# Kernel tuning notes

Measured on AMD Instinct MI355X. Metric: run time of the kernel, lower is better.

Reference implementation:

```python
import jax, jax.numpy as jnp
import numpy as np

B, S, D, H = 2, 2048, 1024, 16
DH = D // H
NEG = jnp.float32(-1e30)


def setup_inputs() -> dict:
    key = jax.random.key(0)
    ks = jax.random.split(key, 5)
    x = jax.random.normal(ks[0], (B, S, D), dtype=jnp.float32)
    # causal mask: attn_mask == 0 means blocked (matches masked_fill(attn_mask == 0))
    attn_mask = jnp.tril(jnp.ones((S, S), dtype=jnp.int32))
    key_padding_mask = jnp.zeros((B, S), dtype=bool)  # True = pad (none here)
    sd = 1.0 / np.sqrt(D)
    W_qkv = jax.random.normal(ks[1], (D, 3 * D), dtype=jnp.float32) * sd
    b_qkv = jnp.zeros((3 * D,), dtype=jnp.float32)
    W_proj = jax.random.normal(ks[2], (D, D), dtype=jnp.float32) * sd
    b_proj = jnp.zeros((D,), dtype=jnp.float32)
    return {"x": x, "W_qkv": W_qkv, "b_qkv": b_qkv, "W_proj": W_proj,
            "b_proj": b_proj, "attn_mask": attn_mask,
            "key_padding_mask": key_padding_mask}


def reference(x, W_qkv, b_qkv, W_proj, b_proj, attn_mask, key_padding_mask):
    scale = jnp.float32(DH) ** -0.5
    qkv = (x @ W_qkv + b_qkv).reshape(B, S, 3, H, DH)
    qkv = jnp.transpose(qkv, (2, 0, 3, 1, 4))  # (3, B, H, S, DH)
    q, k, v = qkv[0], qkv[1], qkv[2]
    attn = jnp.einsum("bhqd,bhkd->bhqk", q, k) * scale  # (B,H,S,S)
    # key padding mask: True -> -inf on that key column
    attn = jnp.where(key_padding_mask[:, None, None, :], NEG, attn)
    # attn mask: 0 -> blocked
    attn = jnp.where(attn_mask[None, None, :, :] == 0, NEG, attn)
    attn = jax.nn.softmax(attn, axis=-1)
    out = jnp.einsum("bhqk,bhkd->bhqd", attn, v)
    out = jnp.transpose(out, (0, 2, 1, 3)).reshape(B, S, D)
    return out @ W_proj + b_proj
```

## Files before the change

### kernel.cpp

```cpp
#include <hip/hip_runtime.h>


typedef __bf16 bf16;
typedef bf16 bf16x4 __attribute__((ext_vector_type(4)));
typedef bf16 bf16x8 __attribute__((ext_vector_type(8)));
typedef float f32x4 __attribute__((ext_vector_type(4)));

#define S_LEN 2048
#define DMODEL 1024
#define NHEAD 16
#define DHEAD 64

__device__ __forceinline__ void async_ld16(void* lds, const void* g) {
  __builtin_amdgcn_global_load_lds(
      (const __attribute__((address_space(1))) unsigned int*)g,
      (__attribute__((address_space(3))) unsigned int*)lds, 16, 0, 0);
}

__global__ __launch_bounds__(256) void convert_f32_bf16(
    const float* __restrict__ in, bf16* __restrict__ out, int n4) {
  int i = blockIdx.x * blockDim.x + threadIdx.x;
  if (i < n4) {
    float4 v = ((const float4*)in)[i];
    bf16x4 o;
    o[0] = (bf16)v.x; o[1] = (bf16)v.y; o[2] = (bf16)v.z; o[3] = (bf16)v.w;
    *(bf16x4*)(&out[4 * i]) = o;
  }
}

__global__ __launch_bounds__(256) void transpose_f32_bf16(
    const float* __restrict__ in, bf16* __restrict__ out, int R, int C) {
  __shared__ float t[32][33];
  int bc = blockIdx.x * 32, br = blockIdx.y * 32;
  int tx = threadIdx.x, ty = threadIdx.y;
#pragma unroll
  for (int i = 0; i < 32; i += 8)
    t[ty + i][tx] = in[(size_t)(br + ty + i) * C + bc + tx];
  __syncthreads();
#pragma unroll
  for (int i = 0; i < 32; i += 8)
    out[(size_t)(bc + ty + i) * R + br + tx] = (bf16)t[tx][ty + i];
}

__global__ __launch_bounds__(256) void gemm_qkv(
    const bf16* __restrict__ A, const bf16* __restrict__ Bt,
    const float* __restrict__ bias, bf16* __restrict__ Oq,
    bf16* __restrict__ Ok, bf16* __restrict__ Ov, int Ksz) {
  __shared__ bf16 As[128 * 32];
  __shared__ bf16 Bs[128 * 32];
  const int tid = threadIdx.x, lane = tid & 63, w = tid >> 6;
  const int wm = (w >> 1) * 64, wn = (w & 1) * 64;
  const int lr = lane & 15, kg = lane >> 4;
  const int m0 = blockIdx.y * 128, n0 = blockIdx.x * 128;

  f32x4 acc[4][4] = {};

  for (int k0 = 0; k0 < Ksz; k0 += 32) {
#pragma unroll
    for (int i = 0; i < 2; ++i) {
      int seg = tid + i * 256;
      int row = seg >> 2, cs = (seg & 3) * 8;
      async_ld16(&As[row * 32 + cs], &A[(size_t)(m0 + row) * Ksz + k0 + cs]);
      async_ld16(&Bs[row * 32 + cs], &Bt[(size_t)(n0 + row) * Ksz + k0 + cs]);
    }
    __syncthreads();
    bf16x8 af[4], bfr[4];
#pragma unroll
    for (int i = 0; i < 4; ++i)
      af[i] = *(const bf16x8*)(&As[(wm + i * 16 + lr) * 32 + kg * 8]);
#pragma unroll
    for (int j = 0; j < 4; ++j)
      bfr[j] = *(const bf16x8*)(&Bs[(wn + j * 16 + lr) * 32 + kg * 8]);
#pragma unroll
    for (int i = 0; i < 4; ++i)
#pragma unroll
      for (int j = 0; j < 4; ++j)
        acc[i][j] = __builtin_amdgcn_mfma_f32_16x16x32_bf16(af[i], bfr[j], acc[i][j], 0, 0, 0);
    __syncthreads();
  }

  const int rbase = kg * 4;
#pragma unroll
  for (int i = 0; i < 4; ++i) {
#pragma unroll
    for (int j = 0; j < 4; ++j) {
      int ncol = n0 + wn + j * 16 + lr;
      float bv = bias[ncol];
#pragma unroll
      for (int r = 0; r < 4; ++r) {
        int m = m0 + wm + i * 16 + rbase + r;
        float v = acc[i][j][r] + bv;
        int t = ncol >> 10, rem = ncol & 1023;
        int h = rem >> 6, d = rem & 63;
        int s = m & 2047;
        size_t hb = (size_t)((m >> 11) * NHEAD + h) * S_LEN;
        if (t == 0)      Oq[(hb + s) * DHEAD + d] = (bf16)v;
        else if (t == 1) Ok[(hb + s) * DHEAD + d] = (bf16)v;
        else             Ov[hb * DHEAD + (size_t)d * S_LEN + s] = (bf16)v;
      }
    }
  }
}

__global__ __launch_bounds__(256) void gemm_proj(
    const bf16* __restrict__ A, const bf16* __restrict__ Bt,
    const float* __restrict__ bias, float* __restrict__ Of,
    int Ksz, int Nsz) {
  __shared__ bf16 As[64 * 32];
  __shared__ bf16 Bs[128 * 32];
  const int tid = threadIdx.x, lane = tid & 63, w = tid >> 6;
  const int wm = (w >> 1) * 32, wn = (w & 1) * 64;
  const int lr = lane & 15, kg = lane >> 4;
  const int m0 = blockIdx.y * 64, n0 = blockIdx.x * 128;

  f32x4 acc[2][4] = {};

  for (int k0 = 0; k0 < Ksz; k0 += 32) {
    {
      int row = tid >> 2, cs = (tid & 3) * 8;
      async_ld16(&As[row * 32 + cs], &A[(size_t)(m0 + row) * Ksz + k0 + cs]);
    }
#pragma unroll
    for (int i = 0; i < 2; ++i) {
      int seg = tid + i * 256;
      int row = seg >> 2, cs = (seg & 3) * 8;
      async_ld16(&Bs[row * 32 + cs], &Bt[(size_t)(n0 + row) * Ksz + k0 + cs]);
    }
    __syncthreads();
    bf16x8 af[2], bfr[4];
#pragma unroll
    for (int i = 0; i < 2; ++i)
      af[i] = *(const bf16x8*)(&As[(wm + i * 16 + lr) * 32 + kg * 8]);
#pragma unroll
    for (int j = 0; j < 4; ++j)
      bfr[j] = *(const bf16x8*)(&Bs[(wn + j * 16 + lr) * 32 + kg * 8]);
#pragma unroll
    for (int i = 0; i < 2; ++i)
#pragma unroll
      for (int j = 0; j < 4; ++j)
        acc[i][j] = __builtin_amdgcn_mfma_f32_16x16x32_bf16(af[i], bfr[j], acc[i][j], 0, 0, 0);
    __syncthreads();
  }

  const int rbase = kg * 4;
#pragma unroll
  for (int i = 0; i < 2; ++i) {
#pragma unroll
    for (int j = 0; j < 4; ++j) {
      int ncol = n0 + wn + j * 16 + lr;
      float bv = bias[ncol];
#pragma unroll
      for (int r = 0; r < 4; ++r) {
        int m = m0 + wm + i * 16 + rbase + r;
        Of[(size_t)m * Nsz + ncol] = acc[i][j][r] + bv;
      }
    }
  }
}

__global__ __launch_bounds__(256) void attn_kernel(
    const bf16* __restrict__ Q, const bf16* __restrict__ K,
    const bf16* __restrict__ Vtg, bf16* __restrict__ O) {
  __shared__ bf16 Ks[128 * 72];
  __shared__ bf16 Vt[64 * 136];
  __shared__ bf16 Pt[4][16 * 136];

  const int tid = threadIdx.x, lane = tid & 63, w = tid >> 6;
  const int lr = lane & 15, quad = lane >> 4;
  const int bh = blockIdx.y;
  const int b = bh >> 4, h = bh & 15;
  const bf16* Qp = Q + (size_t)bh * S_LEN * DHEAD;
  const bf16* Kp = K + (size_t)bh * S_LEN * DHEAD;
  const bf16* Vp = Vtg + (size_t)bh * S_LEN * DHEAD;

  const float qs = 0.125f * 1.44269504f;

  for (int seg = 0; seg < 2; ++seg) {
    const int qt = seg ? (31 - (int)blockIdx.x) : (int)blockIdx.x;
    const int q0 = qt * 64;
    const int qrow = q0 + w * 16;

    bf16x8 q0r = *(const bf16x8*)(Qp + (size_t)(qrow + lr) * DHEAD + quad * 8);
    bf16x8 q1r = *(const bf16x8*)(Qp + (size_t)(qrow + lr) * DHEAD + 32 + quad * 8);
    bf16x8 qf0, qf1;
#pragma unroll
    for (int e = 0; e < 8; ++e) {
      qf0[e] = (bf16)((float)q0r[e] * qs);
      qf1[e] = (bf16)((float)q1r[e] * qs);
    }

    f32x4 acc[4] = {};
    float m_i = -1e30f, l_i = 0.f;

    const int ktiles = (q0 + 63) / 128 + 1;
    for (int kt = 0; kt < ktiles; ++kt) {
      const int kb = kt * 128;
#pragma unroll
      for (int i = 0; i < 4; ++i) {
        int sg = tid + i * 256;
        int krow = sg >> 3, kc = (sg & 7) * 8;
        *(bf16x8*)(&Ks[krow * 72 + kc]) =
            *(const bf16x8*)(&Kp[(size_t)(kb + krow) * DHEAD + kc]);
        int vd = sg >> 4, vs = (sg & 15) * 8;
        *(bf16x8*)(&Vt[vd * 136 + vs]) =
            *(const bf16x8*)(&Vp[(size_t)vd * S_LEN + kb + vs]);
      }
      __syncthreads();

      f32x4 sc[8];
#pragma unroll
      for (int ct = 0; ct < 8; ++ct) {
        bf16x8 kf0 = *(const bf16x8*)(&Ks[(ct * 16 + lr) * 72 + quad * 8]);
        bf16x8 kf1 = *(const bf16x8*)(&Ks[(ct * 16 + lr) * 72 + 32 + quad * 8]);
        f32x4 a = {};
        a = __builtin_amdgcn_mfma_f32_16x16x32_bf16(kf0, qf0, a, 0, 0, 0);
        a = __builtin_amdgcn_mfma_f32_16x16x32_bf16(kf1, qf1, a, 0, 0, 0);
        sc[ct] = a;
      }

      const bool full = (kb + 127) <= qrow;
      float pmax = -1e30f;
      if (full) {
#pragma unroll
        for (int ct = 0; ct < 8; ++ct)
#pragma unroll
          for (int r = 0; r < 4; ++r) pmax = fmaxf(pmax, sc[ct][r]);
      } else {
        const int qg = qrow + lr;
#pragma unroll
        for (int ct = 0; ct < 8; ++ct)
#pragma unroll
          for (int r = 0; r < 4; ++r) {
            int key = kb + ct * 16 + quad * 4 + r;
            if (key > qg) sc[ct][r] = -1e30f;
            pmax = fmaxf(pmax, sc[ct][r]);
          }
      }
      pmax = fmaxf(pmax, __shfl_xor(pmax, 16));
      pmax = fmaxf(pmax, __shfl_xor(pmax, 32));

      float mn = fmaxf(m_i, pmax);
      float alpha = __builtin_amdgcn_exp2f(m_i - mn);
      m_i = mn;
      float psum = 0.f;
#pragma unroll
      for (int ct = 0; ct < 8; ++ct)
#pragma unroll
        for (int r = 0; r < 4; ++r) {
          float p = __builtin_amdgcn_exp2f(sc[ct][r] - mn);
          sc[ct][r] = p;
          psum += p;
        }
      psum += __shfl_xor(psum, 16);
      psum += __shfl_xor(psum, 32);
      l_i = l_i * alpha + psum;
#pragma unroll
      for (int nt = 0; nt < 4; ++nt)
#pragma unroll
        for (int r = 0; r < 4; ++r) acc[nt][r] *= alpha;

#pragma unroll
      for (int ct = 0; ct < 8; ++ct) {
        bf16x4 pk;
#pragma unroll
        for (int r = 0; r < 4; ++r) pk[r] = (bf16)sc[ct][r];
        *(bf16x4*)(&Pt[w][lr * 136 + ct * 16 + quad * 4]) = pk;
      }

#pragma unroll
      for (int k0 = 0; k0 < 4; ++k0) {
        bf16x8 pf = *(const bf16x8*)(&Pt[w][lr * 136 + k0 * 32 + quad * 8]);
#pragma unroll
        for (int nt = 0; nt < 4; ++nt) {
          bf16x8 vf = *(const bf16x8*)(&Vt[(nt * 16 + lr) * 136 + k0 * 32 + quad * 8]);
          acc[nt] = __builtin_amdgcn_mfma_f32_16x16x32_bf16(vf, pf, acc[nt], 0, 0, 0);
        }
      }
      __syncthreads();
    }

    float inv = 1.f / l_i;
    size_t base = ((size_t)(b * S_LEN + qrow + lr)) * DMODEL + h * DHEAD;
#pragma unroll
    for (int nt = 0; nt < 4; ++nt) {
      bf16x4 ov;
#pragma unroll
      for (int r = 0; r < 4; ++r) ov[r] = (bf16)(acc[nt][r] * inv);
      *(bf16x4*)(&O[base + nt * 16 + quad * 4]) = ov;
    }
  }
}

extern "C" void kernel_launch(void* const* d_in, const int* in_sizes, int n_in,
                              void* d_out, int out_size, void* d_ws, size_t ws_size,
                              hipStream_t stream) {
  (void)in_sizes; (void)n_in; (void)out_size; (void)ws_size;
  const float* x     = (const float*)d_in[0];
  const float* Wqkv  = (const float*)d_in[1];
  const float* bqkv  = (const float*)d_in[2];
  const float* Wproj = (const float*)d_in[3];
  const float* bproj = (const float*)d_in[4];
  float* out = (float*)d_out;

  char* ws = (char*)d_ws;
  bf16* Xb  = (bf16*)(ws + 0);
  bf16* AO  = (bf16*)(ws + 0);
  bf16* Wtq = (bf16*)(ws + 8388608);
  bf16* Wtp = (bf16*)(ws + 16777216);
  bf16* Qb  = (bf16*)(ws + 18874368);
  bf16* Kb  = (bf16*)(ws + 27262976);
  bf16* Vtg = (bf16*)(ws + 35651584);

  convert_f32_bf16<<<4096, 256, 0, stream>>>(x, Xb, 4194304 / 4);
  transpose_f32_bf16<<<dim3(96, 32), dim3(32, 8), 0, stream>>>(Wqkv, Wtq, 1024, 3072);
  transpose_f32_bf16<<<dim3(32, 32), dim3(32, 8), 0, stream>>>(Wproj, Wtp, 1024, 1024);
  gemm_qkv<<<dim3(24, 32), 256, 0, stream>>>(Xb, Wtq, bqkv, Qb, Kb, Vtg, 1024);
  attn_kernel<<<dim3(16, 32), 256, 0, stream>>>(Qb, Kb, Vtg, AO);
  gemm_proj<<<dim3(8, 64), 256, 0, stream>>>(AO, Wtp, bproj, out, 1024, 1024);
}
```

Baseline: 215.6 us.

## Merge prep kernels, compute softmax row sums via MFMA, swizzle attention grid

Three conversion and transpose launches are merged into one prep kernel with a block-range dispatch, removing two launch overheads. In attention, the row-sum of probabilities is now computed by an extra MFMA against a ones-row appended to the V tile in LDS, replacing the per-tile cross-lane shuffle reductions. The attention grid is also flattened and remapped so groups of 8 heads share query-tile indices, which may improve L2 locality. The row-sum MFMA adds LDS usage and one MFMA per k-step, and it accumulates the bf16-rounded probabilities, which changes numerics slightly.

```diff
diff --git a/kernel.cpp b/kernel.cpp
--- a/kernel.cpp
+++ b/kernel.cpp
@@ -17,22 +17,30 @@
       (__attribute__((address_space(3))) unsigned int*)lds, 16, 0, 0);
 }
 
-__global__ __launch_bounds__(256) void convert_f32_bf16(
-    const float* __restrict__ in, bf16* __restrict__ out, int n4) {
-  int i = blockIdx.x * blockDim.x + threadIdx.x;
-  if (i < n4) {
-    float4 v = ((const float4*)in)[i];
+__global__ __launch_bounds__(256) void prep_kernel(
+    const float* __restrict__ x, const float* __restrict__ Wq,
+    const float* __restrict__ Wp, bf16* __restrict__ Xb,
+    bf16* __restrict__ Wtq, bf16* __restrict__ Wtp) {
+  __shared__ float t[32][33];
+  const int bid = blockIdx.x, tid = threadIdx.x;
+  if (bid < 4096) {
+    int i = bid * 256 + tid;
+    float4 v = ((const float4*)x)[i];
     bf16x4 o;
     o[0] = (bf16)v.x; o[1] = (bf16)v.y; o[2] = (bf16)v.z; o[3] = (bf16)v.w;
-    *(bf16x4*)(&out[4 * i]) = o;
-  }
-}
-
-__global__ __launch_bounds__(256) void transpose_f32_bf16(
-    const float* __restrict__ in, bf16* __restrict__ out, int R, int C) {
-  __shared__ float t[32][33];
-  int bc = blockIdx.x * 32, br = blockIdx.y * 32;
-  int tx = threadIdx.x, ty = threadIdx.y;
+    *(bf16x4*)(&Xb[4 * i]) = o;
+    return;
+  }
+  const float* in; bf16* out; int R, C, bx, by;
+  if (bid < 7168) {
+    int b = bid - 4096; in = Wq; out = Wtq; R = 1024; C = 3072;
+    bx = b % 96; by = b / 96;
+  } else {
+    int b = bid - 7168; in = Wp; out = Wtp; R = 1024; C = 1024;
+    bx = b % 32; by = b / 32;
+  }
+  int tx = tid & 31, ty = tid >> 5;
+  int bc = bx * 32, br = by * 32;
 #pragma unroll
   for (int i = 0; i < 32; i += 8)
     t[ty + i][tx] = in[(size_t)(br + ty + i) * C + bc + tx];
@@ -162,21 +170,29 @@
     const bf16* __restrict__ Q, const bf16* __restrict__ K,
     const bf16* __restrict__ Vtg, bf16* __restrict__ O) {
   __shared__ bf16 Ks[128 * 72];
-  __shared__ bf16 Vt[64 * 136];
+  __shared__ bf16 Vt[80 * 136];
   __shared__ bf16 Pt[4][16 * 136];
 
   const int tid = threadIdx.x, lane = tid & 63, w = tid >> 6;
   const int lr = lane & 15, quad = lane >> 4;
-  const int bh = blockIdx.y;
+  const int flat = blockIdx.x;
+  const int p = (flat >> 3) & 15;
+  const int bh = (flat & 7) + ((flat >> 7) << 3);
   const int b = bh >> 4, h = bh & 15;
   const bf16* Qp = Q + (size_t)bh * S_LEN * DHEAD;
   const bf16* Kp = K + (size_t)bh * S_LEN * DHEAD;
   const bf16* Vp = Vtg + (size_t)bh * S_LEN * DHEAD;
 
+  for (int i = tid; i < 16 * 136; i += 256) {
+    int rr = i / 136;
+    Vt[(64 + rr) * 136 + (i - rr * 136)] = (rr == 0) ? (bf16)1.0f : (bf16)0.0f;
+  }
+  __syncthreads();
+
   const float qs = 0.125f * 1.44269504f;
 
   for (int seg = 0; seg < 2; ++seg) {
-    const int qt = seg ? (31 - (int)blockIdx.x) : (int)blockIdx.x;
+    const int qt = seg ? (31 - p) : p;
     const int q0 = qt * 64;
     const int qrow = q0 + w * 16;
 
@@ -190,7 +206,8 @@
     }
 
     f32x4 acc[4] = {};
-    float m_i = -1e30f, l_i = 0.f;
+    f32x4 acc5 = {};
+    float m_i = -1e30f;
 
     const int ktiles = (q0 + 63) / 128 + 1;
     for (int kt = 0; kt < ktiles; ++kt) {
@@ -242,22 +259,17 @@
       float mn = fmaxf(m_i, pmax);
       float alpha = __builtin_amdgcn_exp2f(m_i - mn);
       m_i = mn;
-      float psum = 0.f;
 #pragma unroll
       for (int ct = 0; ct < 8; ++ct)
 #pragma unroll
-        for (int r = 0; r < 4; ++r) {
-          float p = __builtin_amdgcn_exp2f(sc[ct][r] - mn);
-          sc[ct][r] = p;
-          psum += p;
-        }
-      psum += __shfl_xor(psum, 16);
-      psum += __shfl_xor(psum, 32);
-      l_i = l_i * alpha + psum;
+        for (int r = 0; r < 4; ++r)
+          sc[ct][r] = __builtin_amdgcn_exp2f(sc[ct][r] - mn);
 #pragma unroll
       for (int nt = 0; nt < 4; ++nt)
 #pragma unroll
         for (int r = 0; r < 4; ++r) acc[nt][r] *= alpha;
+#pragma unroll
+      for (int r = 0; r < 4; ++r) acc5[r] *= alpha;
 
 #pragma unroll
       for (int ct = 0; ct < 8; ++ct) {
@@ -275,11 +287,14 @@
           bf16x8 vf = *(const bf16x8*)(&Vt[(nt * 16 + lr) * 136 + k0 * 32 + quad * 8]);
           acc[nt] = __builtin_amdgcn_mfma_f32_16x16x32_bf16(vf, pf, acc[nt], 0, 0, 0);
         }
+        bf16x8 vf5 = *(const bf16x8*)(&Vt[(64 + lr) * 136 + k0 * 32 + quad * 8]);
+        acc5 = __builtin_amdgcn_mfma_f32_16x16x32_bf16(vf5, pf, acc5, 0, 0, 0);
       }
       __syncthreads();
     }
 
-    float inv = 1.f / l_i;
+    float lsum = __shfl(acc5[0], lr);
+    float inv = 1.f / lsum;
     size_t base = ((size_t)(b * S_LEN + qrow + lr)) * DMODEL + h * DHEAD;
 #pragma unroll
     for (int nt = 0; nt < 4; ++nt) {
@@ -311,10 +326,8 @@
   bf16* Kb  = (bf16*)(ws + 27262976);
   bf16* Vtg = (bf16*)(ws + 35651584);
 
-  convert_f32_bf16<<<4096, 256, 0, stream>>>(x, Xb, 4194304 / 4);
-  transpose_f32_bf16<<<dim3(96, 32), dim3(32, 8), 0, stream>>>(Wqkv, Wtq, 1024, 3072);
-  transpose_f32_bf16<<<dim3(32, 32), dim3(32, 8), 0, stream>>>(Wproj, Wtp, 1024, 1024);
+  prep_kernel<<<8192, 256, 0, stream>>>(x, Wqkv, Wproj, Xb, Wtq, Wtp);
   gemm_qkv<<<dim3(24, 32), 256, 0, stream>>>(Xb, Wtq, bqkv, Qb, Kb, Vtg, 1024);
-  attn_kernel<<<dim3(16, 32), 256, 0, stream>>>(Qb, Kb, Vtg, AO);
+  attn_kernel<<<512, 256, 0, stream>>>(Qb, Kb, Vtg, AO);
   gemm_proj<<<dim3(8, 64), 256, 0, stream>>>(AO, Wtp, bproj, out, 1024, 1024);
 }
```

Measured after the change: 207.6 us. -3.7%, faster.
